# Kernel optimization log

Measured on AMD Instinct MI355X. Metric: run time of the kernel, lower is better.

## Reference

```python
import jax, jax.numpy as jnp
import numpy as np

N, C, G, H = 262144, 512, 16, 16   # nodes, channels, groups, half_group_c
GH = G * H                          # 256
CH_HID = 64                         # channel_mlp hidden = max(GH//4, 8)
SP_HID = 8                          # space_mlp hidden = max(H//4, 8)
B = 1024                            # number of graphs
TEMP = 1.0
EPS = 1e-5


def setup_inputs() -> dict:
    k = jax.random.key(0)
    ks = jax.random.split(k, 20)
    s = 0.02
    rn = lambda kk, sh: jax.random.normal(kk, sh, dtype=jnp.float32)
    return {
        "x": rn(ks[0], (N, C)),
        "batch": jnp.sort(jax.random.randint(ks[1], (N,), 0, B, dtype=jnp.int32)),
        "num_segments": B,
        "cweight": s * rn(ks[2], (1, H)),
        "cbias": 1.0 + s * rn(ks[3], (1, H)),
        "sweight": s * rn(ks[4], (1, H)),
        "sbias": 1.0 + s * rn(ks[5], (1, H)),
        "ch_W1": rn(ks[6], (2 * GH, CH_HID)) / np.sqrt(2 * GH),
        "ch_b1": s * rn(ks[7], (CH_HID,)),
        "ch_W2": rn(ks[8], (CH_HID, GH)) / np.sqrt(CH_HID),
        "ch_b2": s * rn(ks[9], (GH,)),
        "gn_weight": 1.0 + s * rn(ks[10], (GH,)),
        "gn_bias": s * rn(ks[11], (GH,)),
        "sp_W1": rn(ks[12], (3 * H, SP_HID)) / np.sqrt(3 * H),
        "sp_b1": s * rn(ks[13], (SP_HID,)),
        "sp_W2": rn(ks[14], (SP_HID, H)) / np.sqrt(SP_HID),
        "sp_b2": s * rn(ks[15], (H,)),
        "init_scale": jnp.float32(0.1),
        "gnorm_weight": 1.0 + s * rn(ks[16], (C,)),
        "gnorm_bias": s * rn(ks[17], (C,)),
        "gnorm_mean_scale": 1.0 + s * rn(ks[18], (C,)),
    }


def reference(x, batch, num_segments, cweight, cbias, sweight, sbias,
              ch_W1, ch_b1, ch_W2, ch_b2, gn_weight, gn_bias,
              sp_W1, sp_b1, sp_W2, sp_b2, init_scale,
              gnorm_weight, gnorm_bias, gnorm_mean_scale):
    n = x.shape[0]
    xg = x.reshape(n, G, 2 * H)
    x_c = xg[:, :, :H]                      # [N, G, H] channel branch
    x_s = xg[:, :, H:]                      # [N, G, H] spatial branch
    xcf = x_c.reshape(n, GH)

    # --- segment mean / max pooling over graphs ---
    cnt = jax.ops.segment_sum(jnp.ones((n,), x.dtype), batch, num_segments)  # [B]
    gap_mean = jax.ops.segment_sum(xcf, batch, num_segments) / jnp.maximum(cnt, 1.0)[:, None]
    gap_max = jax.ops.segment_max(xcf, batch, num_segments)
    gap_max = jnp.where(cnt[:, None] > 0, gap_max, 0.0)    # empty graphs -> 0
    gap_cat = jnp.concatenate([gap_mean, gap_max], axis=1)  # [B, 2*GH]

    # --- channel gate MLP ---
    hch = jax.nn.relu(gap_cat @ ch_W1 + ch_b1)
    ch_gate = jax.nn.sigmoid((hch @ ch_W2 + ch_b2).reshape(-1, G, H) / TEMP)
    ch_gate = ch_gate * (1.0 + cweight.reshape(1, 1, H)) + cbias.reshape(1, 1, H)
    x_c = x_c * ch_gate[batch]

    # --- GroupNorm over each group's H channels (spatial extent 1) ---
    mu = x_s.mean(axis=2, keepdims=True)
    var = ((x_s - mu) ** 2).mean(axis=2, keepdims=True)
    xn = (x_s - mu) / jnp.sqrt(var + EPS)
    xn = xn * gn_weight.reshape(1, G, H) + gn_bias.reshape(1, G, H)

    # --- spatial context across groups (std is unbiased, ddof=1) ---
    mean_ctx = xn.mean(axis=1)
    max_ctx = xn.max(axis=1)
    std_ctx = jnp.sqrt(((xn - mean_ctx[:, None, :]) ** 2).sum(axis=1) / (G - 1))
    sc = jnp.concatenate([mean_ctx, max_ctx, std_ctx], axis=-1)  # [N, 3H]
    hs = jax.nn.relu(sc @ sp_W1 + sp_b1)
    sp_gate = jax.nn.sigmoid((hs @ sp_W2 + sp_b2).reshape(n, 1, H) / TEMP)
    sp_gate = sp_gate * (1.0 + sweight.reshape(1, 1, H)) + sbias.reshape(1, 1, H)
    x_s = x_s * sp_gate

    # stack -> [N,G,H,2] -> permute -> [N,G,2,H] -> [N,C]
    out = jnp.stack([x_c, x_s], axis=-1).transpose(0, 1, 3, 2).reshape(n, C)
    out = out + jnp.tanh(init_scale) * x

    # --- GraphNorm (PyG): per-graph, per-channel ---
    inv_cnt = 1.0 / jnp.maximum(cnt, 1.0)[:, None]
    gmean = jax.ops.segment_sum(out, batch, num_segments) * inv_cnt
    outc = out - gmean[batch] * gnorm_mean_scale
    gvar = jax.ops.segment_sum(outc * outc, batch, num_segments) * inv_cnt
    out = gnorm_weight * outc / jnp.sqrt(gvar + EPS)[batch] + gnorm_bias

    # channel shuffle with groups=2
    return out.reshape(n, 2, C // 2).transpose(0, 2, 1).reshape(n, C)
```

## Files before the change

### kernel.cpp

```cpp
#include <hip/hip_runtime.h>
#include <hip/hip_bf16.h>
#include <math.h>

#define NN 262144
#define CC 512
#define BB 1024
#define EPSF 1e-5f
#define CAP 512

typedef float f32x4 __attribute__((ext_vector_type(4)));

__device__ __forceinline__ int lower_bound_i(const int* __restrict__ a, int n, int v) {
    int lo = 0, hi = n;
    while (lo < hi) { int mid = (lo + hi) >> 1; if (a[mid] < v) lo = mid + 1; else hi = mid; }
    return lo;
}

__device__ __forceinline__ float sigmoidf(float v) { return 1.0f / (1.0f + __expf(-v)); }

template<int CTRL>
__device__ __forceinline__ float dppAdd(float v) {
    int t = __builtin_amdgcn_update_dpp(0, __float_as_int(v), CTRL, 0xf, 0xf, true);
    return v + __int_as_float(t);
}
template<int CTRL>
__device__ __forceinline__ float dppMax(float v) {
    int t = __builtin_amdgcn_update_dpp(0, __float_as_int(v), CTRL, 0xf, 0xf, true);
    return fmaxf(v, __int_as_float(t));
}

__global__ __launch_bounds__(512, 1) void kFused(
    const float* __restrict__ x, const int* __restrict__ batch,
    const float* __restrict__ cweight, const float* __restrict__ cbias,
    const float* __restrict__ sweight, const float* __restrict__ sbias,
    const float* __restrict__ ch_W1, const float* __restrict__ ch_b1,
    const float* __restrict__ ch_W2, const float* __restrict__ ch_b2,
    const float* __restrict__ gn_w, const float* __restrict__ gn_b,
    const float* __restrict__ sp_W1, const float* __restrict__ sp_b1,
    const float* __restrict__ sp_W2, const float* __restrict__ sp_b2,
    const float* __restrict__ init_scale,
    const float* __restrict__ gms, const float* __restrict__ gw,
    const float* __restrict__ gb,
    float* __restrict__ spgOv, float* __restrict__ out)
{
    __shared__ float red[8][5][256];
    __shared__ float segA[5][256];
    __shared__ float spgL[CAP * 16];
    __shared__ float gap[512];
    __shared__ float part[8][64];
    __shared__ float hch[64];
    __shared__ float cA[512];
    __shared__ float oA[512];

    const int tid  = threadIdx.x;
    const int lane = tid & 63;
    const int w    = tid >> 6;
    const int g    = lane & 15;
    const int q    = lane >> 4;
    const int h0   = q * 4;
    const int kk   = g & 7;
    const float tau = tanhf(init_scale[0]);

    float gwv[4], gbv[4], b2v[4], swv[4], sbv[4], w1m[4], w1x[4], w1s[4], w2r[4];
#pragma unroll
    for (int j = 0; j < 4; ++j) {
        const int h = h0 + j;
        gwv[j] = gn_w[g * 16 + h];
        gbv[j] = gn_b[g * 16 + h];
        b2v[j] = sp_b2[h];
        swv[j] = sweight[h];
        sbv[j] = sbias[h];
        w1m[j] = sp_W1[h * 8 + kk];
        w1x[j] = sp_W1[(16 + h) * 8 + kk];
        w1s[j] = sp_W1[(32 + h) * 8 + kk];
        w2r[j] = sp_W2[kk * 16 + h];
    }
    const float b1k = sp_b1[kk];

    const int l2 = lane * 2;
    const int p0 = (lane >> 3) & 1;

    for (int r = 0; r < 4; ++r) {
        const int b = blockIdx.x * 4 + r;
        const int s = lower_bound_i(batch, NN, b);
        const int e = lower_bound_i(batch, NN, b + 1);
        const int cnt = e - s;

        __syncthreads();

        float sc1[4] = {0.f,0.f,0.f,0.f}, sc2[4] = {0.f,0.f,0.f,0.f};
        float st1[4] = {0.f,0.f,0.f,0.f}, st2[4] = {0.f,0.f,0.f,0.f};
        float mxc[4] = {-INFINITY,-INFINITY,-INFINITY,-INFINITY};

        for (int n = s + w; n < e; n += 8) {
            const float* row = x + (size_t)n * CC + g * 32 + h0;
            const float4 c4 = *(const float4*)row;
            const float4 s4 = *(const float4*)(row + 16);
            float ca[4] = {c4.x, c4.y, c4.z, c4.w};
            float sa[4] = {s4.x, s4.y, s4.z, s4.w};

#pragma unroll
            for (int j = 0; j < 4; ++j) {
                sc1[j] += ca[j];
                sc2[j] = fmaf(ca[j], ca[j], sc2[j]);
                mxc[j] = fmaxf(mxc[j], ca[j]);
            }

            float ls = sa[0] + sa[1] + sa[2] + sa[3];
            float lq = fmaf(sa[0], sa[0], fmaf(sa[1], sa[1], fmaf(sa[2], sa[2], sa[3] * sa[3])));
            ls += __shfl_xor(ls, 16); ls += __shfl_xor(ls, 32);
            lq += __shfl_xor(lq, 16); lq += __shfl_xor(lq, 32);
            const float mu   = ls * 0.0625f;
            const float var  = lq * 0.0625f - mu * mu;
            const float rstd = rsqrtf(var + EPSF);
            float xn[4];
#pragma unroll
            for (int j = 0; j < 4; ++j)
                xn[j] = fmaf((sa[j] - mu) * rstd, gwv[j], gbv[j]);

            float sm[4], mx[4];
#pragma unroll
            for (int j = 0; j < 4; ++j) {
                float v = xn[j];
                v = dppAdd<0xB1>(v); v = dppAdd<0x4E>(v);
                v = dppAdd<0x124>(v); v = dppAdd<0x128>(v);
                sm[j] = v;
                float m = xn[j];
                m = dppMax<0xB1>(m); m = dppMax<0x4E>(m);
                m = dppMax<0x124>(m); m = dppMax<0x128>(m);
                mx[j] = m;
            }
            float mean[4], ssq[4];
#pragma unroll
            for (int j = 0; j < 4; ++j) {
                mean[j] = sm[j] * 0.0625f;
                const float d = xn[j] - mean[j];
                float v = d * d;
                v = dppAdd<0xB1>(v); v = dppAdd<0x4E>(v);
                v = dppAdd<0x124>(v); v = dppAdd<0x128>(v);
                ssq[j] = v;
            }
            float stdc[4];
#pragma unroll
            for (int j = 0; j < 4; ++j) stdc[j] = sqrtf(ssq[j] * (1.0f / 15.0f));

            float p = 0.f;
#pragma unroll
            for (int j = 0; j < 4; ++j) {
                p = fmaf(mean[j], w1m[j], p);
                p = fmaf(mx[j],   w1x[j], p);
                p = fmaf(stdc[j], w1s[j], p);
            }
            p += __shfl_xor(p, 16); p += __shfl_xor(p, 32);
            const float hsk = fmaxf(p + b1k, 0.0f);

            float spg[4];
#pragma unroll
            for (int j = 0; j < 4; ++j) {
                float t = hsk * w2r[j];
                t = dppAdd<0xB1>(t); t = dppAdd<0x4E>(t); t = dppAdd<0x141>(t);
                spg[j] = fmaf(sigmoidf(t + b2v[j]), 1.0f + swv[j], sbv[j]) + tau;
            }

#pragma unroll
            for (int j = 0; j < 4; ++j) {
                const float os = spg[j] * sa[j];
                st1[j] += os;
                st2[j] = fmaf(os, os, st2[j]);
            }

            if (g == 0) {
                const int idx = n - s;
                if (idx < CAP)
                    *(float4*)(&spgL[idx * 16 + h0]) = make_float4(spg[0], spg[1], spg[2], spg[3]);
                else
                    *(float4*)(spgOv + (size_t)n * 16 + h0) = make_float4(spg[0], spg[1], spg[2], spg[3]);
            }
        }

        const int ch = g * 16 + h0;
        *(float4*)&red[w][0][ch] = make_float4(sc1[0], sc1[1], sc1[2], sc1[3]);
        *(float4*)&red[w][1][ch] = make_float4(mxc[0], mxc[1], mxc[2], mxc[3]);
        *(float4*)&red[w][2][ch] = make_float4(sc2[0], sc2[1], sc2[2], sc2[3]);
        *(float4*)&red[w][3][ch] = make_float4(st1[0], st1[1], st1[2], st1[3]);
        *(float4*)&red[w][4][ch] = make_float4(st2[0], st2[1], st2[2], st2[3]);
        __syncthreads();
        if (tid < 256) {
            float a0 = 0.f, a2 = 0.f, a3 = 0.f, a4 = 0.f, a1 = -INFINITY;
#pragma unroll
            for (int ww = 0; ww < 8; ++ww) {
                a0 += red[ww][0][tid];
                a1 = fmaxf(a1, red[ww][1][tid]);
                a2 += red[ww][2][tid];
                a3 += red[ww][3][tid];
                a4 += red[ww][4][tid];
            }
            segA[0][tid] = a0; segA[1][tid] = a1; segA[2][tid] = a2;
            segA[3][tid] = a3; segA[4][tid] = a4;
        }
        __syncthreads();

        const float inv = 1.0f / (float)max(cnt, 1);
        if (tid < 256) {
            gap[tid] = segA[0][tid] * inv;
            gap[256 + tid] = (cnt > 0) ? segA[1][tid] : 0.0f;
        }
        __syncthreads();
        {
            const int t = tid & 63, pp = tid >> 6;
            float acc = 0.f;
            for (int i = pp * 64; i < pp * 64 + 64; ++i)
                acc = fmaf(gap[i], ch_W1[i * 64 + t], acc);
            part[pp][t] = acc;
        }
        __syncthreads();
        if (tid < 64) {
            float a = ch_b1[tid];
#pragma unroll
            for (int pp = 0; pp < 8; ++pp) a += part[pp][tid];
            hch[tid] = fmaxf(a, 0.0f);
        }
        __syncthreads();
        if (tid < 256) {
            const int c = tid, gg = c >> 4, h = c & 15;
            float acc = ch_b2[c];
            for (int k = 0; k < 64; ++k) acc = fmaf(hch[k], ch_W2[k * 256 + c], acc);
            const float chg = fmaf(sigmoidf(acc), 1.0f + cweight[h], cbias[h]);
            const float ct = chg + tau;
            const int colc = gg * 32 + h, cols = colc + 16;
            {
                const float S1 = segA[0][c], S2 = segA[2][c];
                const float m  = ct * S1 * inv;
                const float e2 = ct * ct * S2 * inv;
                const float smv = gms[colc];
                const float gv = fmaxf(e2 - m * m * smv * (2.0f - smv), 0.0f);
                const float A  = gw[colc] * rsqrtf(gv + EPSF);
                cA[colc] = A * ct;
                oA[colc] = gb[colc] - m * smv * A;
            }
            {
                const float T1 = segA[3][c], T2 = segA[4][c];
                const float m  = T1 * inv;
                const float e2 = T2 * inv;
                const float smv = gms[cols];
                const float gv = fmaxf(e2 - m * m * smv * (2.0f - smv), 0.0f);
                const float A  = gw[cols] * rsqrtf(gv + EPSF);
                cA[cols] = A;
                oA[cols] = gb[cols] - m * smv * A;
            }
        }
        __syncthreads();

        const float cf0 = cA[l2],       cf1 = cA[l2 + 1];
        const float cf2 = cA[128 + l2], cf3 = cA[129 + l2];
        const float cf4 = cA[256 + l2], cf5 = cA[257 + l2];
        const float cf6 = cA[384 + l2], cf7 = cA[385 + l2];
        const float of0 = oA[l2],       of1 = oA[l2 + 1];
        const float of2 = oA[128 + l2], of3 = oA[129 + l2];
        const float of4 = oA[256 + l2], of5 = oA[257 + l2];
        const float of6 = oA[384 + l2], of7 = oA[385 + l2];

        for (int n = s + w; n < e; n += 8) {
            const float2* r2 = (const float2*)(x + (size_t)n * CC);
            const float2 xa = r2[lane];
            const float2 xb = r2[64 + lane];
            const float2 xc = r2[128 + lane];
            const float2 xd = r2[192 + lane];
            const int idx = n - s;
            float2 sp;
            if (idx < CAP) sp = *(const float2*)(&spgL[idx * 16 + (l2 & 15)]);
            else           sp = *(const float2*)(spgOv + (size_t)n * 16 + (l2 & 15));
            const float me = p0 ? sp.x : 1.0f;
            const float mo = p0 ? sp.y : 1.0f;

            const float v0 = fmaf(cf0 * me, xa.x, of0);
            const float v1 = fmaf(cf1 * mo, xa.y, of1);
            const float v2 = fmaf(cf2 * me, xb.x, of2);
            const float v3 = fmaf(cf3 * mo, xb.y, of3);
            const float v4 = fmaf(cf4 * me, xc.x, of4);
            const float v5 = fmaf(cf5 * mo, xc.y, of5);
            const float v6 = fmaf(cf6 * me, xd.x, of6);
            const float v7 = fmaf(cf7 * mo, xd.y, of7);

            f32x4* o4 = (f32x4*)(out + (size_t)n * CC);
            f32x4 pa = {v0, v4, v1, v5};
            f32x4 pb = {v2, v6, v3, v7};
            __builtin_nontemporal_store(pa, &o4[lane]);
            __builtin_nontemporal_store(pb, &o4[64 + lane]);
        }
    }
}

extern "C" void kernel_launch(void* const* d_in, const int* in_sizes, int n_in,
                              void* d_out, int out_size, void* d_ws, size_t ws_size,
                              hipStream_t stream) {
    (void)in_sizes; (void)n_in; (void)out_size; (void)ws_size;
    const float* x        = (const float*)d_in[0];
    const int*   batch    = (const int*)d_in[1];
    const float* cweight  = (const float*)d_in[3];
    const float* cbias    = (const float*)d_in[4];
    const float* sweight  = (const float*)d_in[5];
    const float* sbias    = (const float*)d_in[6];
    const float* ch_W1    = (const float*)d_in[7];
    const float* ch_b1    = (const float*)d_in[8];
    const float* ch_W2    = (const float*)d_in[9];
    const float* ch_b2    = (const float*)d_in[10];
    const float* gn_w     = (const float*)d_in[11];
    const float* gn_b     = (const float*)d_in[12];
    const float* sp_W1    = (const float*)d_in[13];
    const float* sp_b1    = (const float*)d_in[14];
    const float* sp_W2    = (const float*)d_in[15];
    const float* sp_b2    = (const float*)d_in[16];
    const float* init_sc  = (const float*)d_in[17];
    const float* gnw      = (const float*)d_in[18];
    const float* gnb      = (const float*)d_in[19];
    const float* gms      = (const float*)d_in[20];

    float* spgOv = (float*)d_ws;
    float* outp  = (float*)d_out;

    kFused<<<BB / 4, 512, 0, stream>>>(x, batch, cweight, cbias, sweight, sbias,
                                       ch_W1, ch_b1, ch_W2, ch_b2, gn_w, gn_b,
                                       sp_W1, sp_b1, sp_W2, sp_b2, init_sc,
                                       gms, gnw, gnb, spgOv, outp);
}
```

Before: 502.4 us.

## Cut LDS footprint with shared atomics, raise occupancy, prefetch rows, halve graphs per block

Replaces the per-wave 8x5x256 LDS reduction buffer with shared-memory atomic accumulators, using an order-preserving uint encoding for the max. This shrinks LDS use so launch bounds can request 4 blocks per CU. The grid doubles by processing 2 graphs per block instead of 4, and both node loops software-prefetch the next row into registers. The intent is more resident waves and latency hiding for a memory-bound pass, at the cost of LDS atomic contention, nondeterministic float summation order, and higher register pressure.

New measurement: 595.6 us. +18.6%, slower.

```diff
diff --git a/kernel.cpp b/kernel.cpp
--- a/kernel.cpp
+++ b/kernel.cpp
@@ -18,6 +18,14 @@
 
 __device__ __forceinline__ float sigmoidf(float v) { return 1.0f / (1.0f + __expf(-v)); }
 
+__device__ __forceinline__ unsigned fenc(float f) {
+    unsigned b = __float_as_uint(f);
+    return (b & 0x80000000u) ? ~b : (b | 0x80000000u);
+}
+__device__ __forceinline__ float fdec(unsigned k) {
+    return __uint_as_float((k & 0x80000000u) ? (k & 0x7fffffffu) : ~k);
+}
+
 template<int CTRL>
 __device__ __forceinline__ float dppAdd(float v) {
     int t = __builtin_amdgcn_update_dpp(0, __float_as_int(v), CTRL, 0xf, 0xf, true);
@@ -29,7 +37,7 @@
     return fmaxf(v, __int_as_float(t));
 }
 
-__global__ __launch_bounds__(512, 1) void kFused(
+__global__ __launch_bounds__(512, 4) void kFused(
     const float* __restrict__ x, const int* __restrict__ batch,
     const float* __restrict__ cweight, const float* __restrict__ cbias,
     const float* __restrict__ sweight, const float* __restrict__ sbias,
@@ -43,14 +51,14 @@
     const float* __restrict__ gb,
     float* __restrict__ spgOv, float* __restrict__ out)
 {
-    __shared__ float red[8][5][256];
-    __shared__ float segA[5][256];
-    __shared__ float spgL[CAP * 16];
-    __shared__ float gap[512];
-    __shared__ float part[8][64];
-    __shared__ float hch[64];
-    __shared__ float cA[512];
-    __shared__ float oA[512];
+    __shared__ float    segS1[256], segS2[256], segT1[256], segT2[256];
+    __shared__ unsigned segM[256];
+    __shared__ float    spgL[CAP * 16];
+    __shared__ float    gap[512];
+    __shared__ float    part[8][64];
+    __shared__ float    hch[64];
+    __shared__ float    cA[512];
+    __shared__ float    oA[512];
 
     const int tid  = threadIdx.x;
     const int lane = tid & 63;
@@ -80,22 +88,42 @@
     const int l2 = lane * 2;
     const int p0 = (lane >> 3) & 1;
 
-    for (int r = 0; r < 4; ++r) {
-        const int b = blockIdx.x * 4 + r;
+    for (int r = 0; r < 2; ++r) {
+        const int b = blockIdx.x * 2 + r;
         const int s = lower_bound_i(batch, NN, b);
         const int e = lower_bound_i(batch, NN, b + 1);
         const int cnt = e - s;
 
         __syncthreads();
+        if (tid < 256) {
+            segS1[tid] = 0.f; segS2[tid] = 0.f;
+            segT1[tid] = 0.f; segT2[tid] = 0.f;
+            segM[tid] = fenc(-INFINITY);
+        }
+        __syncthreads();
 
         float sc1[4] = {0.f,0.f,0.f,0.f}, sc2[4] = {0.f,0.f,0.f,0.f};
         float st1[4] = {0.f,0.f,0.f,0.f}, st2[4] = {0.f,0.f,0.f,0.f};
         float mxc[4] = {-INFINITY,-INFINITY,-INFINITY,-INFINITY};
 
-        for (int n = s + w; n < e; n += 8) {
-            const float* row = x + (size_t)n * CC + g * 32 + h0;
-            const float4 c4 = *(const float4*)row;
-            const float4 s4 = *(const float4*)(row + 16);
+        float4 c4, s4;
+        {
+            const int n = s + w;
+            if (n < e) {
+                const float* row = x + (size_t)n * CC + g * 32 + h0;
+                c4 = *(const float4*)row;
+                s4 = *(const float4*)(row + 16);
+            }
+        }
+        for (int n = s + w; n < e; ) {
+            const int nn = n + 8;
+            float4 c4n, s4n;
+            if (nn < e) {
+                const float* row = x + (size_t)nn * CC + g * 32 + h0;
+                c4n = *(const float4*)row;
+                s4n = *(const float4*)(row + 16);
+            }
+
             float ca[4] = {c4.x, c4.y, c4.z, c4.w};
             float sa[4] = {s4.x, s4.y, s4.z, s4.w};
 
@@ -176,34 +204,28 @@
                 else
                     *(float4*)(spgOv + (size_t)n * 16 + h0) = make_float4(spg[0], spg[1], spg[2], spg[3]);
             }
-        }
-
-        const int ch = g * 16 + h0;
-        *(float4*)&red[w][0][ch] = make_float4(sc1[0], sc1[1], sc1[2], sc1[3]);
-        *(float4*)&red[w][1][ch] = make_float4(mxc[0], mxc[1], mxc[2], mxc[3]);
-        *(float4*)&red[w][2][ch] = make_float4(sc2[0], sc2[1], sc2[2], sc2[3]);
-        *(float4*)&red[w][3][ch] = make_float4(st1[0], st1[1], st1[2], st1[3]);
-        *(float4*)&red[w][4][ch] = make_float4(st2[0], st2[1], st2[2], st2[3]);
-        __syncthreads();
-        if (tid < 256) {
-            float a0 = 0.f, a2 = 0.f, a3 = 0.f, a4 = 0.f, a1 = -INFINITY;
-#pragma unroll
-            for (int ww = 0; ww < 8; ++ww) {
-                a0 += red[ww][0][tid];
-                a1 = fmaxf(a1, red[ww][1][tid]);
-                a2 += red[ww][2][tid];
-                a3 += red[ww][3][tid];
-                a4 += red[ww][4][tid];
-            }
-            segA[0][tid] = a0; segA[1][tid] = a1; segA[2][tid] = a2;
-            segA[3][tid] = a3; segA[4][tid] = a4;
+
+            c4 = c4n; s4 = s4n;
+            n = nn;
+        }
+
+        {
+            const int ch = g * 16 + h0;
+#pragma unroll
+            for (int j = 0; j < 4; ++j) {
+                atomicAdd(&segS1[ch + j], sc1[j]);
+                atomicAdd(&segS2[ch + j], sc2[j]);
+                atomicAdd(&segT1[ch + j], st1[j]);
+                atomicAdd(&segT2[ch + j], st2[j]);
+                atomicMax(&segM[ch + j], fenc(mxc[j]));
+            }
         }
         __syncthreads();
 
         const float inv = 1.0f / (float)max(cnt, 1);
         if (tid < 256) {
-            gap[tid] = segA[0][tid] * inv;
-            gap[256 + tid] = (cnt > 0) ? segA[1][tid] : 0.0f;
+            gap[tid] = segS1[tid] * inv;
+            gap[256 + tid] = (cnt > 0) ? fdec(segM[tid]) : 0.0f;
         }
         __syncthreads();
         {
@@ -229,7 +251,7 @@
             const float ct = chg + tau;
             const int colc = gg * 32 + h, cols = colc + 16;
             {
-                const float S1 = segA[0][c], S2 = segA[2][c];
+                const float S1 = segS1[c], S2 = segS2[c];
                 const float m  = ct * S1 * inv;
                 const float e2 = ct * ct * S2 * inv;
                 const float smv = gms[colc];
@@ -239,7 +261,7 @@
                 oA[colc] = gb[colc] - m * smv * A;
             }
             {
-                const float T1 = segA[3][c], T2 = segA[4][c];
+                const float T1 = segT1[c], T2 = segT2[c];
                 const float m  = T1 * inv;
                 const float e2 = T2 * inv;
                 const float smv = gms[cols];
@@ -260,16 +282,30 @@
         const float of4 = oA[256 + l2], of5 = oA[257 + l2];
         const float of6 = oA[384 + l2], of7 = oA[385 + l2];
 
-        for (int n = s + w; n < e; n += 8) {
-            const float2* r2 = (const float2*)(x + (size_t)n * CC);
-            const float2 xa = r2[lane];
-            const float2 xb = r2[64 + lane];
-            const float2 xc = r2[128 + lane];
-            const float2 xd = r2[192 + lane];
-            const int idx = n - s;
-            float2 sp;
-            if (idx < CAP) sp = *(const float2*)(&spgL[idx * 16 + (l2 & 15)]);
-            else           sp = *(const float2*)(spgOv + (size_t)n * 16 + (l2 & 15));
+        float2 xa, xb, xc, xd, sp;
+        {
+            const int n = s + w;
+            if (n < e) {
+                const float2* r2 = (const float2*)(x + (size_t)n * CC);
+                xa = r2[lane]; xb = r2[64 + lane];
+                xc = r2[128 + lane]; xd = r2[192 + lane];
+                const int idx = n - s;
+                sp = (idx < CAP) ? *(const float2*)(&spgL[idx * 16 + (l2 & 15)])
+                                 : *(const float2*)(spgOv + (size_t)n * 16 + (l2 & 15));
+            }
+        }
+        for (int n = s + w; n < e; ) {
+            const int nn = n + 8;
+            float2 xa2, xb2, xc2, xd2, sp2;
+            if (nn < e) {
+                const float2* r2 = (const float2*)(x + (size_t)nn * CC);
+                xa2 = r2[lane]; xb2 = r2[64 + lane];
+                xc2 = r2[128 + lane]; xd2 = r2[192 + lane];
+                const int idx = nn - s;
+                sp2 = (idx < CAP) ? *(const float2*)(&spgL[idx * 16 + (l2 & 15)])
+                                  : *(const float2*)(spgOv + (size_t)nn * 16 + (l2 & 15));
+            }
+
             const float me = p0 ? sp.x : 1.0f;
             const float mo = p0 ? sp.y : 1.0f;
 
@@ -287,6 +323,9 @@
             f32x4 pb = {v2, v6, v3, v7};
             __builtin_nontemporal_store(pa, &o4[lane]);
             __builtin_nontemporal_store(pb, &o4[64 + lane]);
+
+            xa = xa2; xb = xb2; xc = xc2; xd = xd2; sp = sp2;
+            n = nn;
         }
     }
 }
@@ -319,7 +358,7 @@
     float* spgOv = (float*)d_ws;
     float* outp  = (float*)d_out;
 
-    kFused<<<BB / 4, 512, 0, stream>>>(x, batch, cweight, cbias, sweight, sbias,
+    kFused<<<BB / 2, 512, 0, stream>>>(x, batch, cweight, cbias, sweight, sbias,
                                        ch_W1, ch_b1, ch_W2, ch_b2, gn_w, gn_b,
                                        sp_W1, sp_b1, sp_W2, sp_b2, init_sc,
                                        gms, gnw, gnb, spgOv, outp);
```
